# Kernel tuning notes

Measured on AMD Instinct MI355X. Metric: run time of the kernel, lower is better.

The kernel has to match this reference:

```python
import jax, jax.numpy as jnp
import numpy as np

B, T, N = 512, 64, 30
F_IN, D, C = 512, 256, 7


def setup_inputs() -> dict:
    key = jax.random.key(0)
    ks = jax.random.split(key, 9)
    return {
        "real": jax.random.normal(ks[0], (B, N, F_IN), dtype=jnp.float32),
        "imag": jax.random.normal(ks[1], (B, N, F_IN), dtype=jnp.float32),  # ignored by forward
        "graph_sigs": jax.random.uniform(ks[2], (B, T, N, N), dtype=jnp.float32),
        # DiGCNConv params (glorot-ish weight, zero bias like default init)
        "W": jax.random.normal(ks[3], (F_IN, D), dtype=jnp.float32) / np.sqrt(F_IN),
        "conv_bias": jnp.zeros((D,), dtype=jnp.float32),
        # pool_lin: Linear(D, 1), bias initialized to zero in the module
        "pool_w": jax.random.normal(ks[4], (D,), dtype=jnp.float32) / np.sqrt(D),
        "pool_b": jnp.zeros((), dtype=jnp.float32),
        # head: Conv1d(N, C, kernel_size=1) == dense [C, N] matmul over node scores
        "head_w": jax.random.normal(ks[5], (C, N), dtype=jnp.float32) / np.sqrt(N),
        "head_b": jax.random.normal(ks[6], (C,), dtype=jnp.float32) * 0.01,
    }


def reference(real, imag, graph_sigs, W, conv_bias, pool_w, pool_b, head_w, head_b):
    # Per-graph adjacency: mean over the T signal slices (dominant memory traffic).
    adj = jnp.mean(graph_sigs, axis=1)                      # [B, N, N]
    # DiGCNConv: x @ W, then edge-weighted scatter-add out[dst] += w(src,dst) * xW[src]
    # which for a dense adjacency is exactly adj^T @ xW, plus bias.
    xw = jnp.einsum('bnf,fd->bnd', real, W)                 # [B, N, D]
    agg = jnp.einsum('bij,bid->bjd', adj, xw) + conv_bias   # [B, N, D]
    h = jax.nn.relu(agg)
    # pool_lin -> per-node scalar score
    node_score = jnp.einsum('bnd,d->bn', h, pool_w) + pool_b  # [B, N]
    # Conv1d(N, C, k=1) on [1, N, 1] == node_score @ head_w.T + head_b
    logits = node_score @ head_w.T + head_b                 # [B, C]
    return jax.nn.softmax(logits, axis=-1)
```

## Files before the change

### kernel.cpp

```cpp
#include <hip/hip_runtime.h>

typedef float f32x4 __attribute__((ext_vector_type(4)));

#define B_  512
#define T_  64
#define N_  30
#define FIN 512
#define D_  256
#define C_  7

__global__ __launch_bounds__(256, 2)
void digcn_fused(const float* __restrict__ real,
                 const float* __restrict__ gs,
                 const float* __restrict__ W,
                 const float* __restrict__ conv_bias,
                 const float* __restrict__ pool_w,
                 const float* __restrict__ pool_b,
                 const float* __restrict__ head_w,
                 const float* __restrict__ head_b,
                 float* __restrict__ out)
{
    __shared__ __align__(16) float lds[17536];
    float* adjS   = lds + 16384;
    float* scoreS = lds + 17344;
    float* sumS   = lds + 17472;
    float* logitS = lds + 17504;

    const int tid  = threadIdx.x;
    const int b    = blockIdx.x;
    const int w    = tid >> 6;
    const int l    = tid & 63;
    const int c0   = l * 4;
    const int row0 = w * 8;

    const float* realb = real + (size_t)b * (N_ * FIN);
    const float* gsb   = gs   + (size_t)b * (T_ * N_ * N_);

    #pragma unroll
    for (int it = 0; it < 16; ++it) {
        int idx = (it * 256 + tid) * 4;
        f32x4 v = (f32x4){0.f, 0.f, 0.f, 0.f};
        if (idx < N_ * FIN) v = *(const f32x4*)(realb + idx);
        *(f32x4*)(lds + idx) = v;
    }
    __syncthreads();

    f32x4 acc[8];
    #pragma unroll
    for (int rr = 0; rr < 8; ++rr) acc[rr] = (f32x4){0.f, 0.f, 0.f, 0.f};
    float adjacc[4] = {0.f, 0.f, 0.f, 0.f};

    float pg[4];
    #pragma unroll
    for (int r = 0; r < 4; ++r) {
        int e = tid + r * 256;
        pg[r] = (e < N_ * N_) ? gsb[e] : 0.f;
    }

    for (int ts = 0; ts < T_; ++ts) {
        float ng[4] = {0.f, 0.f, 0.f, 0.f};
        if (ts < T_ - 1) {
            #pragma unroll
            for (int r = 0; r < 4; ++r) {
                int e = tid + r * 256;
                ng[r] = (e < N_ * N_) ? gsb[(ts + 1) * (N_ * N_) + e] : 0.f;
            }
        }
        #pragma unroll
        for (int half = 0; half < 2; ++half) {
            const int f = ts * 8 + half * 4;
            f32x4 wv[4];
            #pragma unroll
            for (int k = 0; k < 4; ++k)
                wv[k] = *(const f32x4*)(W + (f + k) * D_ + c0);
            #pragma unroll
            for (int rr = 0; rr < 8; ++rr) {
                f32x4 rv = *(const f32x4*)(lds + (row0 + rr) * FIN + f);
                #pragma unroll
                for (int k = 0; k < 4; ++k)
                    acc[rr] += wv[k] * rv[k];
            }
        }
        #pragma unroll
        for (int r = 0; r < 4; ++r) adjacc[r] += pg[r];
        #pragma unroll
        for (int r = 0; r < 4; ++r) pg[r] = ng[r];
    }
    __syncthreads();

    #pragma unroll
    for (int r = 0; r < 4; ++r) {
        int e = tid + r * 256;
        if (e < N_ * N_) {
            int i = e / N_;
            int j = e - i * N_;
            adjS[i * 32 + j] = adjacc[r] * (1.f / (float)T_);
        }
    }
    if (tid < 60) adjS[(tid >> 1) * 32 + 30 + (tid & 1)] = 0.f;
    #pragma unroll
    for (int rr = 0; rr < 8; ++rr) {
        int row = row0 + rr;
        if (row < N_) *(f32x4*)(lds + row * D_ + c0) = acc[rr];
    }
    __syncthreads();

    float xcol[N_];
    #pragma unroll
    for (int i = 0; i < N_; ++i) xcol[i] = lds[i * D_ + tid];
    const float bias = conv_bias[tid];
    const float pw   = pool_w[tid];

    #pragma unroll
    for (int j0 = 0; j0 < N_; j0 += 4) {
        f32x4 agg = (f32x4){0.f, 0.f, 0.f, 0.f};
        #pragma unroll
        for (int i = 0; i < N_; ++i) {
            f32x4 a4 = *(const f32x4*)(adjS + i * 32 + j0);
            agg += a4 * xcol[i];
        }
        #pragma unroll
        for (int c = 0; c < 4; ++c) {
            float h = agg[c] + bias;
            h = h > 0.f ? h : 0.f;
            float v = h * pw;
            #pragma unroll
            for (int m = 32; m >= 1; m >>= 1) v += __shfl_xor(v, m, 64);
            if (l == 0) scoreS[w * 32 + j0 + c] = v;
        }
    }
    __syncthreads();

    if (tid < N_)
        sumS[tid] = scoreS[tid] + scoreS[32 + tid] + scoreS[64 + tid] + scoreS[96 + tid]
                  + pool_b[0];
    __syncthreads();
    if (tid < C_) {
        float lg = head_b[tid];
        #pragma unroll
        for (int j = 0; j < N_; ++j) lg += sumS[j] * head_w[tid * N_ + j];
        logitS[tid] = lg;
    }
    __syncthreads();
    if (tid < C_) {
        float m = logitS[0];
        #pragma unroll
        for (int c = 1; c < C_; ++c) m = fmaxf(m, logitS[c]);
        float s = 0.f;
        #pragma unroll
        for (int c = 0; c < C_; ++c) s += expf(logitS[c] - m);
        out[b * C_ + tid] = expf(logitS[tid] - m) / s;
    }
}

extern "C" void kernel_launch(void* const* d_in, const int* in_sizes, int n_in,
                              void* d_out, int out_size, void* d_ws, size_t ws_size,
                              hipStream_t stream) {
    const float* real      = (const float*)d_in[0];
    const float* gs        = (const float*)d_in[2];
    const float* W         = (const float*)d_in[3];
    const float* conv_bias = (const float*)d_in[4];
    const float* pool_w    = (const float*)d_in[5];
    const float* pool_b    = (const float*)d_in[6];
    const float* head_w    = (const float*)d_in[7];
    const float* head_b    = (const float*)d_in[8];
    float* outp            = (float*)d_out;

    digcn_fused<<<dim3(B_), dim3(256), 0, stream>>>(
        real, gs, W, conv_bias, pool_w, pool_b, head_w, head_b, outp);
}
```

Before: 270.8 us.

## Split FIN reduction across four wave quarters with 512-thread blocks

```diff
diff --git a/kernel.cpp b/kernel.cpp
--- a/kernel.cpp
+++ b/kernel.cpp
@@ -8,8 +8,9 @@
 #define FIN 512
 #define D_  256
 #define C_  7
+#define NN  (N_ * N_)
 
-__global__ __launch_bounds__(256, 2)
+__global__ __launch_bounds__(512, 4)
 void digcn_fused(const float* __restrict__ real,
                  const float* __restrict__ gs,
                  const float* __restrict__ W,
@@ -20,113 +21,137 @@
                  const float* __restrict__ head_b,
                  float* __restrict__ out)
 {
-    __shared__ __align__(16) float lds[17536];
+    __shared__ __align__(16) float lds[17600];
     float* adjS   = lds + 16384;
-    float* scoreS = lds + 17344;
-    float* sumS   = lds + 17472;
-    float* logitS = lds + 17504;
+    float* scoreS = lds + 17408;
+    float* sumS   = lds + 17536;
+    float* logitS = lds + 17568;
 
-    const int tid  = threadIdx.x;
-    const int b    = blockIdx.x;
-    const int w    = tid >> 6;
-    const int l    = tid & 63;
-    const int c0   = l * 4;
-    const int row0 = w * 8;
+    const int tid = threadIdx.x;
+    const int b   = blockIdx.x;
+    const int w   = tid >> 6;
+    const int l   = tid & 63;
+    const int kq  = w & 3;
+    const int rg  = w >> 2;
+    const int rh  = l >> 5;
+    const int cg  = l & 31;
+    const int r0  = rg * 16 + rh * 8;
+    const int c0  = cg * 8;
 
     const float* realb = real + (size_t)b * (N_ * FIN);
-    const float* gsb   = gs   + (size_t)b * (T_ * N_ * N_);
+    const float* gsb   = gs   + (size_t)b * (T_ * NN);
+    const float* WQ    = W + (size_t)(kq * 128) * D_ + c0;
+
+    float pa0 = gsb[tid];
+    float pa1 = (tid + 512 < NN) ? gsb[tid + 512] : 0.f;
+    float pb0 = gsb[NN + tid];
+    float pb1 = (tid + 512 < NN) ? gsb[NN + tid + 512] : 0.f;
 
     #pragma unroll
-    for (int it = 0; it < 16; ++it) {
-        int idx = (it * 256 + tid) * 4;
+    for (int it = 0; it < 8; ++it) {
+        int idx = (it * 512 + tid) * 4;
         f32x4 v = (f32x4){0.f, 0.f, 0.f, 0.f};
         if (idx < N_ * FIN) v = *(const f32x4*)(realb + idx);
         *(f32x4*)(lds + idx) = v;
     }
     __syncthreads();
 
-    f32x4 acc[8];
+    f32x4 acc[8][2];
     #pragma unroll
-    for (int rr = 0; rr < 8; ++rr) acc[rr] = (f32x4){0.f, 0.f, 0.f, 0.f};
-    float adjacc[4] = {0.f, 0.f, 0.f, 0.f};
+    for (int rr = 0; rr < 8; ++rr) {
+        acc[rr][0] = (f32x4){0.f, 0.f, 0.f, 0.f};
+        acc[rr][1] = (f32x4){0.f, 0.f, 0.f, 0.f};
+    }
+    float adj0 = 0.f, adj1 = 0.f;
 
-    float pg[4];
-    #pragma unroll
-    for (int r = 0; r < 4; ++r) {
-        int e = tid + r * 256;
-        pg[r] = (e < N_ * N_) ? gsb[e] : 0.f;
-    }
-
-    for (int ts = 0; ts < T_; ++ts) {
-        float ng[4] = {0.f, 0.f, 0.f, 0.f};
-        if (ts < T_ - 1) {
+    for (int it = 0; it < 32; ++it) {
+        float na0 = 0.f, na1 = 0.f, nb0 = 0.f, nb1 = 0.f;
+        if (it < 31) {
+            const float* g2 = gsb + (2 * it + 2) * NN;
+            na0 = g2[tid];
+            nb0 = g2[NN + tid];
+            if (tid + 512 < NN) { na1 = g2[tid + 512]; nb1 = g2[NN + tid + 512]; }
+        }
+        const float* Wit = WQ + it * 4 * D_;
+        f32x4 wv[4][2];
+        #pragma unroll
+        for (int ff = 0; ff < 4; ++ff) {
+            wv[ff][0] = *(const f32x4*)(Wit + ff * D_);
+            wv[ff][1] = *(const f32x4*)(Wit + ff * D_ + 4);
+        }
+        #pragma unroll
+        for (int rr = 0; rr < 8; ++rr) {
+            f32x4 rv = *(const f32x4*)(lds + (r0 + rr) * FIN + kq * 128 + it * 4);
             #pragma unroll
-            for (int r = 0; r < 4; ++r) {
-                int e = tid + r * 256;
-                ng[r] = (e < N_ * N_) ? gsb[(ts + 1) * (N_ * N_) + e] : 0.f;
+            for (int ff = 0; ff < 4; ++ff) {
+                acc[rr][0] += wv[ff][0] * rv[ff];
+                acc[rr][1] += wv[ff][1] * rv[ff];
             }
         }
-        #pragma unroll
-        for (int half = 0; half < 2; ++half) {
-            const int f = ts * 8 + half * 4;
-            f32x4 wv[4];
-            #pragma unroll
-            for (int k = 0; k < 4; ++k)
-                wv[k] = *(const f32x4*)(W + (f + k) * D_ + c0);
-            #pragma unroll
-            for (int rr = 0; rr < 8; ++rr) {
-                f32x4 rv = *(const f32x4*)(lds + (row0 + rr) * FIN + f);
-                #pragma unroll
-                for (int k = 0; k < 4; ++k)
-                    acc[rr] += wv[k] * rv[k];
-            }
-        }
-        #pragma unroll
-        for (int r = 0; r < 4; ++r) adjacc[r] += pg[r];
-        #pragma unroll
-        for (int r = 0; r < 4; ++r) pg[r] = ng[r];
+        adj0 += pa0 + pb0;
+        adj1 += pa1 + pb1;
+        pa0 = na0; pa1 = na1; pb0 = nb0; pb1 = nb1;
     }
     __syncthreads();
 
-    #pragma unroll
-    for (int r = 0; r < 4; ++r) {
-        int e = tid + r * 256;
-        if (e < N_ * N_) {
-            int i = e / N_;
-            int j = e - i * N_;
-            adjS[i * 32 + j] = adjacc[r] * (1.f / (float)T_);
+    {
+        int i = tid / N_, j = tid - i * N_;
+        adjS[i * 32 + j] = adj0 * (1.f / (float)T_);
+        int e = tid + 512;
+        if (e < NN) {
+            int i2 = e / N_, j2 = e - i2 * N_;
+            adjS[i2 * 32 + j2] = adj1 * (1.f / (float)T_);
         }
     }
     if (tid < 60) adjS[(tid >> 1) * 32 + 30 + (tid & 1)] = 0.f;
+
+    float* xwS = lds;
     #pragma unroll
-    for (int rr = 0; rr < 8; ++rr) {
-        int row = row0 + rr;
-        if (row < N_) *(f32x4*)(lds + row * D_ + c0) = acc[rr];
+    for (int step = 0; step < 4; ++step) {
+        if (kq == step) {
+            #pragma unroll
+            for (int rr = 0; rr < 8; ++rr) {
+                float* p = xwS + (r0 + rr) * D_ + c0;
+                if (step == 0) {
+                    *(f32x4*)p       = acc[rr][0];
+                    *(f32x4*)(p + 4) = acc[rr][1];
+                } else {
+                    f32x4 t0 = *(const f32x4*)p;
+                    f32x4 t1 = *(const f32x4*)(p + 4);
+                    *(f32x4*)p       = t0 + acc[rr][0];
+                    *(f32x4*)(p + 4) = t1 + acc[rr][1];
+                }
+            }
+        }
+        __syncthreads();
     }
-    __syncthreads();
 
-    float xcol[N_];
-    #pragma unroll
-    for (int i = 0; i < N_; ++i) xcol[i] = lds[i * D_ + tid];
-    const float bias = conv_bias[tid];
-    const float pw   = pool_w[tid];
+    if (tid < D_) {
+        float xcol[N_];
+        #pragma unroll
+        for (int i = 0; i < N_; ++i) xcol[i] = xwS[i * D_ + tid];
+        const float bias = conv_bias[tid];
+        const float pw   = pool_w[tid];
 
-    #pragma unroll
-    for (int j0 = 0; j0 < N_; j0 += 4) {
-        f32x4 agg = (f32x4){0.f, 0.f, 0.f, 0.f};
         #pragma unroll
-        for (int i = 0; i < N_; ++i) {
-            f32x4 a4 = *(const f32x4*)(adjS + i * 32 + j0);
-            agg += a4 * xcol[i];
-        }
-        #pragma unroll
-        for (int c = 0; c < 4; ++c) {
-            float h = agg[c] + bias;
-            h = h > 0.f ? h : 0.f;
-            float v = h * pw;
+        for (int j0 = 0; j0 < N_ + 2; j0 += 4) {
+            f32x4 agg = (f32x4){0.f, 0.f, 0.f, 0.f};
             #pragma unroll
-            for (int m = 32; m >= 1; m >>= 1) v += __shfl_xor(v, m, 64);
-            if (l == 0) scoreS[w * 32 + j0 + c] = v;
+            for (int i = 0; i < N_; ++i) {
+                f32x4 a4 = *(const f32x4*)(adjS + i * 32 + j0);
+                agg += a4 * xcol[i];
+            }
+            #pragma unroll
+            for (int c = 0; c < 4; ++c) {
+                if (j0 + c < N_) {
+                    float h = agg[c] + bias;
+                    h = h > 0.f ? h : 0.f;
+                    float v = h * pw;
+                    #pragma unroll
+                    for (int m = 32; m >= 1; m >>= 1) v += __shfl_xor(v, m, 64);
+                    if (l == 0) scoreS[w * 32 + j0 + c] = v;
+                }
+            }
         }
     }
     __syncthreads();
@@ -166,6 +191,6 @@
     const float* head_b    = (const float*)d_in[8];
     float* outp            = (float*)d_out;
 
-    digcn_fused<<<dim3(B_), dim3(256), 0, stream>>>(
+    digcn_fused<<<dim3(B_), dim3(512), 0, stream>>>(
         real, gs, W, conv_bias, pool_w, pool_b, head_w, head_b, outp);
 }
```

After: 281.3 us. +3.9%, slower.

## Split xW matmul across 512 threads with K-split and direct global reads

Applied to the files above, without the earlier changes.

```diff
diff --git a/kernel.cpp b/kernel.cpp
--- a/kernel.cpp
+++ b/kernel.cpp
@@ -8,8 +8,9 @@
 #define FIN 512
 #define D_  256
 #define C_  7
+#define NN  900
 
-__global__ __launch_bounds__(256, 2)
+__global__ __launch_bounds__(512, 4)
 void digcn_fused(const float* __restrict__ real,
                  const float* __restrict__ gs,
                  const float* __restrict__ W,
@@ -20,113 +21,113 @@
                  const float* __restrict__ head_b,
                  float* __restrict__ out)
 {
-    __shared__ __align__(16) float lds[17536];
-    float* adjS   = lds + 16384;
-    float* scoreS = lds + 17344;
-    float* sumS   = lds + 17472;
-    float* logitS = lds + 17504;
+    __shared__ __align__(16) float xwS[N_ * D_];
+    __shared__ __align__(16) float adjS[32 * 32];
+    __shared__ float scoreS[4 * 32];
+    __shared__ float sumS[32];
+    __shared__ float logitS[8];
 
     const int tid  = threadIdx.x;
     const int b    = blockIdx.x;
     const int w    = tid >> 6;
     const int l    = tid & 63;
-    const int c0   = l * 4;
-    const int row0 = w * 8;
+    const int kq   = w & 1;
+    const int g    = (w >> 1) & 1;
+    const int cgrp = w >> 2;
+    const int rh   = l >> 5;
+    const int r0   = g * 14 + rh * 8;
+    const int c0   = cgrp * 128 + (l & 31) * 4;
 
-    const float* realb = real + (size_t)b * (N_ * FIN);
-    const float* gsb   = gs   + (size_t)b * (T_ * N_ * N_);
-
-    #pragma unroll
-    for (int it = 0; it < 16; ++it) {
-        int idx = (it * 256 + tid) * 4;
-        f32x4 v = (f32x4){0.f, 0.f, 0.f, 0.f};
-        if (idx < N_ * FIN) v = *(const f32x4*)(realb + idx);
-        *(f32x4*)(lds + idx) = v;
-    }
-    __syncthreads();
+    const float* realb = real + (size_t)b * (N_ * FIN) + r0 * FIN + kq * 256;
+    const float* gsb   = gs   + (size_t)b * (T_ * NN);
+    const float* Wb    = W + (size_t)(kq * 256) * D_ + c0;
 
     f32x4 acc[8];
     #pragma unroll
     for (int rr = 0; rr < 8; ++rr) acc[rr] = (f32x4){0.f, 0.f, 0.f, 0.f};
-    float adjacc[4] = {0.f, 0.f, 0.f, 0.f};
+    float adj0 = 0.f, adj1 = 0.f;
 
-    float pg[4];
-    #pragma unroll
-    for (int r = 0; r < 4; ++r) {
-        int e = tid + r * 256;
-        pg[r] = (e < N_ * N_) ? gsb[e] : 0.f;
+    float pg0 = gsb[tid];
+    float pg1 = (tid + 512 < NN) ? gsb[tid + 512] : 0.f;
+
+    for (int it = 0; it < 64; ++it) {
+        float ng0 = 0.f, ng1 = 0.f;
+        if (it < 63) {
+            ng0 = gsb[(it + 1) * NN + tid];
+            if (tid + 512 < NN) ng1 = gsb[(it + 1) * NN + tid + 512];
+        }
+        const float* Wit = Wb + it * 4 * D_;
+        f32x4 wv0 = *(const f32x4*)(Wit);
+        f32x4 wv1 = *(const f32x4*)(Wit + D_);
+        f32x4 wv2 = *(const f32x4*)(Wit + 2 * D_);
+        f32x4 wv3 = *(const f32x4*)(Wit + 3 * D_);
+        const float* rp = realb + it * 4;
+        #pragma unroll
+        for (int rr = 0; rr < 8; ++rr) {
+            f32x4 rv = *(const f32x4*)(rp + rr * FIN);
+            acc[rr] += wv0 * rv[0];
+            acc[rr] += wv1 * rv[1];
+            acc[rr] += wv2 * rv[2];
+            acc[rr] += wv3 * rv[3];
+        }
+        adj0 += pg0; adj1 += pg1;
+        pg0 = ng0;  pg1 = ng1;
     }
 
-    for (int ts = 0; ts < T_; ++ts) {
-        float ng[4] = {0.f, 0.f, 0.f, 0.f};
-        if (ts < T_ - 1) {
-            #pragma unroll
-            for (int r = 0; r < 4; ++r) {
-                int e = tid + r * 256;
-                ng[r] = (e < N_ * N_) ? gsb[(ts + 1) * (N_ * N_) + e] : 0.f;
+    {
+        int i = tid / N_, j = tid - i * N_;
+        adjS[i * 32 + j] = adj0 * (1.f / (float)T_);
+        int e = tid + 512;
+        if (e < NN) {
+            int i2 = e / N_, j2 = e - i2 * N_;
+            adjS[i2 * 32 + j2] = adj1 * (1.f / (float)T_);
+        }
+        if (tid < 60) adjS[(tid >> 1) * 32 + 30 + (tid & 1)] = 0.f;
+    }
+    if (kq == 0) {
+        #pragma unroll
+        for (int rr = 0; rr < 8; ++rr)
+            *(f32x4*)(xwS + (r0 + rr) * D_ + c0) = acc[rr];
+    }
+    __syncthreads();
+    if (kq == 1) {
+        #pragma unroll
+        for (int rr = 0; rr < 8; ++rr) {
+            int row = r0 + rr;
+            if (!(g == 1 && row < 16)) {
+                float* p = xwS + row * D_ + c0;
+                *(f32x4*)p = *(const f32x4*)p + acc[rr];
             }
         }
-        #pragma unroll
-        for (int half = 0; half < 2; ++half) {
-            const int f = ts * 8 + half * 4;
-            f32x4 wv[4];
-            #pragma unroll
-            for (int k = 0; k < 4; ++k)
-                wv[k] = *(const f32x4*)(W + (f + k) * D_ + c0);
-            #pragma unroll
-            for (int rr = 0; rr < 8; ++rr) {
-                f32x4 rv = *(const f32x4*)(lds + (row0 + rr) * FIN + f);
-                #pragma unroll
-                for (int k = 0; k < 4; ++k)
-                    acc[rr] += wv[k] * rv[k];
-            }
-        }
-        #pragma unroll
-        for (int r = 0; r < 4; ++r) adjacc[r] += pg[r];
-        #pragma unroll
-        for (int r = 0; r < 4; ++r) pg[r] = ng[r];
     }
     __syncthreads();
 
-    #pragma unroll
-    for (int r = 0; r < 4; ++r) {
-        int e = tid + r * 256;
-        if (e < N_ * N_) {
-            int i = e / N_;
-            int j = e - i * N_;
-            adjS[i * 32 + j] = adjacc[r] * (1.f / (float)T_);
-        }
-    }
-    if (tid < 60) adjS[(tid >> 1) * 32 + 30 + (tid & 1)] = 0.f;
-    #pragma unroll
-    for (int rr = 0; rr < 8; ++rr) {
-        int row = row0 + rr;
-        if (row < N_) *(f32x4*)(lds + row * D_ + c0) = acc[rr];
-    }
-    __syncthreads();
+    if (tid < D_) {
+        float xcol[N_];
+        #pragma unroll
+        for (int i = 0; i < N_; ++i) xcol[i] = xwS[i * D_ + tid];
+        const float bias = conv_bias[tid];
+        const float pw   = pool_w[tid];
 
-    float xcol[N_];
-    #pragma unroll
-    for (int i = 0; i < N_; ++i) xcol[i] = lds[i * D_ + tid];
-    const float bias = conv_bias[tid];
-    const float pw   = pool_w[tid];
-
-    #pragma unroll
-    for (int j0 = 0; j0 < N_; j0 += 4) {
-        f32x4 agg = (f32x4){0.f, 0.f, 0.f, 0.f};
         #pragma unroll
-        for (int i = 0; i < N_; ++i) {
-            f32x4 a4 = *(const f32x4*)(adjS + i * 32 + j0);
-            agg += a4 * xcol[i];
-        }
-        #pragma unroll
-        for (int c = 0; c < 4; ++c) {
-            float h = agg[c] + bias;
-            h = h > 0.f ? h : 0.f;
-            float v = h * pw;
+        for (int j0 = 0; j0 < N_ + 2; j0 += 4) {
+            f32x4 agg = (f32x4){0.f, 0.f, 0.f, 0.f};
             #pragma unroll
-            for (int m = 32; m >= 1; m >>= 1) v += __shfl_xor(v, m, 64);
-            if (l == 0) scoreS[w * 32 + j0 + c] = v;
+            for (int i = 0; i < N_; ++i) {
+                f32x4 a4 = *(const f32x4*)(adjS + i * 32 + j0);
+                agg += a4 * xcol[i];
+            }
+            #pragma unroll
+            for (int c = 0; c < 4; ++c) {
+                if (j0 + c < N_) {
+                    float h = agg[c] + bias;
+                    h = h > 0.f ? h : 0.f;
+                    float v = h * pw;
+                    #pragma unroll
+                    for (int m = 32; m >= 1; m >>= 1) v += __shfl_xor(v, m, 64);
+                    if (l == 0) scoreS[w * 32 + j0 + c] = v;
+                }
+            }
         }
     }
     __syncthreads();
@@ -166,6 +167,6 @@
     const float* head_b    = (const float*)d_in[8];
     float* outp            = (float*)d_out;
 
-    digcn_fused<<<dim3(B_), dim3(256), 0, stream>>>(
+    digcn_fused<<<dim3(B_), dim3(512), 0, stream>>>(
         real, gs, W, conv_bias, pool_w, pool_b, head_w, head_b, outp);
 }
```

Measured after the change: 324.2 us. 19.7% more time.
